# Optimization experiments

Hardware: AMD Instinct MI355X
Metric: run time of the kernel (lower is better)

The kernel has to match this reference:

```python
import jax, jax.numpy as jnp
import numpy as np

B, H, W, C = 4, 64, 64, 256
C8 = C // 8

def setup_inputs() -> dict:
    key = jax.random.key(0)
    k1, k2, k3, k4 = jax.random.split(key, 4)
    # glorot-uniform-ish init for 1x1 conv kernels stored as [Cin, Cout]
    def glorot(k, cin, cout):
        lim = np.sqrt(6.0 / (cin + cout)).astype(np.float32)
        return jax.random.uniform(k, (cin, cout), jnp.float32, -lim, lim)
    return {
        "x": jax.random.normal(k1, (B, H, W, C), jnp.float32),
        "kernel_f": glorot(k2, C, C8),
        "kernel_g": glorot(k3, C, C8),
        "kernel_h": glorot(k4, C, C),
        "gamma": jnp.zeros((1,), jnp.float32),
    }

def reference(x, kernel_f, kernel_g, kernel_h, gamma):
    b, h, w, c = x.shape
    n = h * w
    xf = x.reshape(b, n, c)                       # [B, N, C]
    # 1x1 convs == per-position matmuls
    f = jnp.einsum('bnc,cd->bnd', xf, kernel_f)   # [B, N, C/8]
    g = jnp.einsum('bnc,cd->bnd', xf, kernel_g)   # [B, N, C/8]
    hh = jnp.einsum('bnc,cd->bnd', xf, kernel_h)  # [B, N, C]
    s = jnp.einsum('bnd,bmd->bnm', g, f)          # [B, N, N]
    beta = jax.nn.softmax(s, axis=-1)
    o = jnp.einsum('bnm,bmc->bnc', beta, hh)      # [B, N, C]
    o = o.reshape(b, h, w, c)
    return gamma * o + x
```

## Files before the change

### kernel.cpp

```cpp
#include <hip/hip_runtime.h>
#include <hip/hip_bf16.h>

typedef __bf16 bf16x8 __attribute__((ext_vector_type(8)));
typedef float f32x4 __attribute__((ext_vector_type(4)));
typedef float f32x16 __attribute__((ext_vector_type(16)));
typedef unsigned short u16;
typedef unsigned int u32;
typedef const __attribute__((address_space(1))) u32 gu32;
typedef __attribute__((address_space(3))) u32 lu32;

__device__ __forceinline__ u16 f2bf_rne(float f){
  union { float f; u32 u; } v; v.f = f;
  u32 r = v.u + 0x7fffu + ((v.u >> 16) & 1u);
  return (u16)(r >> 16);
}
__device__ __forceinline__ u32 pack2(float a, float b){
  return __builtin_amdgcn_perm(__float_as_uint(a), __float_as_uint(b), 0x03020706u);
}
__device__ __forceinline__ void stage16(const u16* g, u16* l){
  __builtin_amdgcn_global_load_lds((gu32*)g, (lu32*)l, 16, 0, 0);
}
#define BARRIER_LGKM() asm volatile("s_waitcnt lgkmcnt(0)\n\ts_barrier" ::: "memory")

__global__ __launch_bounds__(256) void prep_kernel(
    const float* __restrict__ Wf, const float* __restrict__ Wg,
    const float* __restrict__ Wh, u16* __restrict__ WcatT){
  __shared__ float tile[32][33];
  const int tx = threadIdx.x & 31, ty = threadIdx.x >> 5;
  const int k0 = blockIdx.x * 32, n0 = blockIdx.y * 32;
  #pragma unroll
  for (int i = 0; i < 4; ++i){
    int k = k0 + ty + i * 8, n = n0 + tx;
    float v;
    if (n < 256)      v = Wh[k * 256 + n];
    else if (n < 288) v = Wf[k * 32 + (n - 256)];
    else              v = Wg[k * 32 + (n - 288)];
    tile[ty + i * 8][tx] = v;
  }
  __syncthreads();
  #pragma unroll
  for (int i = 0; i < 4; ++i){
    int n = n0 + ty + i * 8, k = k0 + tx;
    WcatT[n * 256 + k] = f2bf_rne(tile[tx][ty + i * 8]);
  }
}

__global__ __launch_bounds__(512) void proj_kernel(
    const float* __restrict__ x, const u16* __restrict__ WcatT,
    u16* __restrict__ Qg, u16* __restrict__ Kg, u16* __restrict__ Vfrag)
{
  __shared__ __align__(16) u16 smem[256 * 72];
  u16 (*xb)[264] = (u16(*)[264])smem;
  u16 (*Vr)[72]  = (u16(*)[72])smem;

  const int tid = threadIdx.x;
  const int lane = tid & 63, wave = tid >> 6;
  const int L = lane & 15, quad = lane >> 4;
  const int rowgrp = wave >> 1, colhalf = wave & 1;
  const int n0 = blockIdx.x * 64;

  const float4* xsrc = (const float4*)(x + (size_t)n0 * 256);
  #pragma unroll
  for (int j = 0; j < 8; ++j){
    int idx = j * 512 + tid;
    int row = idx >> 6, col4 = idx & 63;
    float4 v = xsrc[idx];
    u32 p0 = (u32)f2bf_rne(v.x) | ((u32)f2bf_rne(v.y) << 16);
    u32 p1 = (u32)f2bf_rne(v.z) | ((u32)f2bf_rne(v.w) << 16);
    *(uint2*)&xb[row][col4 * 4] = make_uint2(p0, p1);
  }
  __syncthreads();

  f32x4 acc[10];
  #pragma unroll
  for (int cc = 0; cc < 10; ++cc) acc[cc] = (f32x4){0.f, 0.f, 0.f, 0.f};

  #pragma unroll
  for (int kk = 0; kk < 8; ++kk){
    bf16x8 a = *(const bf16x8*)&xb[rowgrp * 16 + L][kk * 32 + quad * 8];
    #pragma unroll
    for (int cc = 0; cc < 10; ++cc){
      int ccg = colhalf * 10 + cc;
      bf16x8 bfr = *(const bf16x8*)(WcatT + (size_t)(ccg * 16 + L) * 256 + kk * 32 + quad * 8);
      acc[cc] = __builtin_amdgcn_mfma_f32_16x16x32_bf16(a, bfr, acc[cc], 0, 0, 0);
    }
  }

  if (colhalf){
    #pragma unroll
    for (int cc = 6; cc < 10; ++cc){
      int ccg = 10 + cc;
      u16* dst = (ccg < 18) ? Kg : Qg;
      float sc = (ccg < 18) ? 1.0f : 1.44269504088896f;
      int c = (ccg & 1) * 16 + L;
      #pragma unroll
      for (int r = 0; r < 4; ++r){
        int row = n0 + rowgrp * 16 + quad * 4 + r;
        dst[(size_t)row * 32 + c] = f2bf_rne(acc[cc][r] * sc);
      }
    }
  }

  __syncthreads();

  {
    const int cmax = colhalf ? 6 : 10;
    for (int cc = 0; cc < cmax; ++cc){
      int ccg = colhalf * 10 + cc;
      int c = ccg * 16 + L;
      #pragma unroll
      for (int r = 0; r < 4; ++r){
        int tn = rowgrp * 16 + quad * 4 + r;
        int p  = ((tn & 15) << 2) | (tn >> 4);
        Vr[c][p] = f2bf_rne(acc[cc][r]);
      }
    }
  }
  __syncthreads();

  u16* Vblk = Vfrag + (size_t)blockIdx.x * (256 * 64);
  #pragma unroll
  for (int i = 0; i < 4; ++i){
    int idx = i * 512 + tid;
    *(uint4*)(Vblk + (size_t)idx * 8) = *(const uint4*)&Vr[idx & 255][(idx >> 8) * 8];
  }
}

__global__ __launch_bounds__(512, 4) void flash_kernel(
    const u16* __restrict__ Qg, const u16* __restrict__ Kg, const u16* __restrict__ Vfrag,
    u16* __restrict__ Opart, float* __restrict__ Lpart)
{
  constexpr float SH = -92.33248261689366f;
  __shared__ __align__(16) u16 Plds[128][72];
  __shared__ __align__(16) u16 Vlds[16384];

  const int tid = threadIdx.x, lane = tid & 63, wave = tid >> 6;
  const int L = lane & 15, quad = lane >> 4;
  const int m32 = lane & 31, h32 = lane >> 5;
  const int qquad = wave & 3, chalf = wave >> 2;
  const int b = blockIdx.y, split = blockIdx.z;
  const int qblk = blockIdx.x * 128;

  const u16* Qb = Qg + (size_t)(b * 4096) * 32;
  const u16* Kb = Kg + (size_t)(b * 4096) * 32;
  const u16* Vb = Vfrag + (size_t)b * (64 * 256 * 64);

  const int g0 = split * 16;
  {
    const u16* vt = Vb + (size_t)g0 * (256 * 64);
    #pragma unroll
    for (int i = 0; i < 4; ++i){
      int chunk = wave * 4 + i;
      stage16(vt + chunk * 512 + lane * 8, &Vlds[chunk * 512]);
    }
  }
  bf16x8 qa = *(const bf16x8*)(Qb + (size_t)(qblk + wave * 16 + L) * 32 + quad * 8);
  const u16* kp0 = Kb + (size_t)(g0 * 64 + L) * 32 + quad * 8;
  bf16x8 kc0 = *(const bf16x8*)(kp0);
  bf16x8 kc1 = *(const bf16x8*)(kp0 + 512);
  bf16x8 kc2 = *(const bf16x8*)(kp0 + 1024);
  bf16x8 kc3 = *(const bf16x8*)(kp0 + 1536);

  f32x16 acc[4];
  #pragma unroll
  for (int ct = 0; ct < 4; ++ct)
    #pragma unroll
    for (int i = 0; i < 16; ++i) acc[ct][i] = 0.f;
  float lsum[4] = {0.f, 0.f, 0.f, 0.f};
  const f32x4 zero = (f32x4){0.f, 0.f, 0.f, 0.f};

  for (int kt = 0; kt < 16; ++kt){
    const int g = g0 + kt;

    f32x4 s0 = __builtin_amdgcn_mfma_f32_16x16x32_bf16(qa, kc0, zero, 0, 0, 0);
    f32x4 s1 = __builtin_amdgcn_mfma_f32_16x16x32_bf16(qa, kc1, zero, 0, 0, 0);
    f32x4 s2 = __builtin_amdgcn_mfma_f32_16x16x32_bf16(qa, kc2, zero, 0, 0, 0);
    f32x4 s3 = __builtin_amdgcn_mfma_f32_16x16x32_bf16(qa, kc3, zero, 0, 0, 0);

    #pragma unroll
    for (int r = 0; r < 4; ++r){
      float p0 = __builtin_amdgcn_exp2f(s0[r] + SH);
      float p1 = __builtin_amdgcn_exp2f(s1[r] + SH);
      float p2 = __builtin_amdgcn_exp2f(s2[r] + SH);
      float p3 = __builtin_amdgcn_exp2f(s3[r] + SH);
      lsum[r] += (p0 + p1) + (p2 + p3);
      *(uint2*)&Plds[wave * 16 + quad * 4 + r][L * 4] =
          make_uint2(pack2(p0, p1), pack2(p2, p3));
    }

    __syncthreads();

    bf16x8 kn0, kn1, kn2, kn3;
    if (kt < 15){
      const u16* kpn = Kb + (size_t)((g + 1) * 64 + L) * 32 + quad * 8;
      kn0 = *(const bf16x8*)(kpn);
      kn1 = *(const bf16x8*)(kpn + 512);
      kn2 = *(const bf16x8*)(kpn + 1024);
      kn3 = *(const bf16x8*)(kpn + 1536);
    }

    #pragma unroll
    for (int ks = 0; ks < 4; ++ks){
      bf16x8 af = *(const bf16x8*)&Plds[qquad * 32 + m32][ks * 16 + h32 * 8];
      const int vbase = ((ks * 2 + h32) * 256 + chalf * 128 + m32) * 8;
      #pragma unroll
      for (int ct = 0; ct < 4; ++ct){
        bf16x8 vf = *(const bf16x8*)&Vlds[vbase + ct * 32 * 8];
        acc[ct] = __builtin_amdgcn_mfma_f32_32x32x16_bf16(af, vf, acc[ct], 0, 0, 0);
      }
    }

    BARRIER_LGKM();

    if (kt < 15){
      const u16* vt = Vb + (size_t)(g + 1) * (256 * 64);
      #pragma unroll
      for (int i = 0; i < 4; ++i){
        int chunk = wave * 4 + i;
        stage16(vt + chunk * 512 + lane * 8, &Vlds[chunk * 512]);
      }
      kc0 = kn0; kc1 = kn1; kc2 = kn2; kc3 = kn3;
    }
  }

  u16* Ob = Opart + ((size_t)split * 16384 + (size_t)b * 4096 + qblk) * 256;
  #pragma unroll
  for (int ct = 0; ct < 4; ++ct){
    #pragma unroll
    for (int rg = 0; rg < 16; ++rg){
      int row = qquad * 32 + (rg & 3) + 8 * (rg >> 2) + 4 * h32;
      int c = chalf * 128 + ct * 32 + m32;
      Ob[(size_t)row * 256 + c] = (u16)(__float_as_uint(acc[ct][rg]) >> 16);
    }
  }
  #pragma unroll
  for (int r = 0; r < 4; ++r){
    lsum[r] += __shfl_xor(lsum[r], 1);
    lsum[r] += __shfl_xor(lsum[r], 2);
    lsum[r] += __shfl_xor(lsum[r], 4);
    lsum[r] += __shfl_xor(lsum[r], 8);
  }
  if (L == 0){
    float* Lp = Lpart + split * 16384 + b * 4096 + qblk + wave * 16;
    #pragma unroll
    for (int r = 0; r < 4; ++r) Lp[quad * 4 + r] = lsum[r];
  }
}

__global__ __launch_bounds__(256) void combine_kernel(
    const float* __restrict__ x, const float* __restrict__ gamma,
    const u16* __restrict__ Opart, const float* __restrict__ Lpart,
    float* __restrict__ out)
{
  const int t = threadIdx.x;
  const int row = blockIdx.x * 8 + (t >> 5);
  const int c0 = (t & 31) * 8;
  const size_t base = (size_t)row * 256 + c0;
  float os[8];
  #pragma unroll
  for (int i = 0; i < 8; ++i) os[i] = 0.f;
  float ls = 0.f;
  #pragma unroll
  for (int s = 0; s < 4; ++s){
    ls += Lpart[s * 16384 + row];
    uint4 u = *(const uint4*)(Opart + (size_t)s * 16384 * 256 + base);
    os[0] += __uint_as_float(u.x << 16);
    os[1] += __uint_as_float(u.x & 0xffff0000u);
    os[2] += __uint_as_float(u.y << 16);
    os[3] += __uint_as_float(u.y & 0xffff0000u);
    os[4] += __uint_as_float(u.z << 16);
    os[5] += __uint_as_float(u.z & 0xffff0000u);
    os[6] += __uint_as_float(u.w << 16);
    os[7] += __uint_as_float(u.w & 0xffff0000u);
  }
  const float r = gamma[0] / ls;
  float4 x0 = *(const float4*)(x + base);
  float4 x1 = *(const float4*)(x + base + 4);
  float4 o0, o1;
  o0.x = os[0] * r + x0.x;  o0.y = os[1] * r + x0.y;
  o0.z = os[2] * r + x0.z;  o0.w = os[3] * r + x0.w;
  o1.x = os[4] * r + x1.x;  o1.y = os[5] * r + x1.y;
  o1.z = os[6] * r + x1.z;  o1.w = os[7] * r + x1.w;
  *(float4*)(out + base)     = o0;
  *(float4*)(out + base + 4) = o1;
}

extern "C" void kernel_launch(void* const* d_in, const int* in_sizes, int n_in,
                              void* d_out, int out_size, void* d_ws, size_t ws_size,
                              hipStream_t stream) {
  const float* x     = (const float*)d_in[0];
  const float* Wf    = (const float*)d_in[1];
  const float* Wg    = (const float*)d_in[2];
  const float* Wh    = (const float*)d_in[3];
  const float* gamma = (const float*)d_in[4];
  float* out = (float*)d_out;

  u16* p = (u16*)d_ws;
  u16* Qg    = p;  p += 16384 * 32;
  u16* Kg    = p;  p += 16384 * 32;
  u16* Vfrag = p;  p += 4 * 64 * 256 * 64;
  u16* WcatT = p;  p += 320 * 256;
  u16* Opart = p;  p += (size_t)4 * 16384 * 256;
  float* Lpart = (float*)p;

  prep_kernel<<<dim3(8, 10), 256, 0, stream>>>(Wf, Wg, Wh, WcatT);
  proj_kernel<<<256, 512, 0, stream>>>(x, WcatT, Qg, Kg, Vfrag);
  flash_kernel<<<dim3(32, 4, 4), 512, 0, stream>>>(Qg, Kg, Vfrag, Opart, Lpart);
  combine_kernel<<<2048, 256, 0, stream>>>(x, gamma, Opart, Lpart, out);
}
```

Before: 161.0 us.

## Read V fragments straight from global and double-buffer P to drop a barrier

The flash kernel no longer stages each V tile into LDS via global_load_lds. Each wave now loads its V fragments directly from global memory, and its output tile changes from 32 rows × 128 columns to a 2×2 block of 64 rows × 64 columns. P goes into a double-buffered LDS array, so one barrier per iteration is enough instead of two, and the next-tile K loads are issued right after the QK MFMAs. This cuts LDS traffic and synchronisation but adds repeated global/L2 reads of V across waves and may expose global load latency ahead of the PV MFMAs.

```diff
diff --git a/kernel.cpp b/kernel.cpp
--- a/kernel.cpp
+++ b/kernel.cpp
@@ -6,8 +6,6 @@
 typedef float f32x16 __attribute__((ext_vector_type(16)));
 typedef unsigned short u16;
 typedef unsigned int u32;
-typedef const __attribute__((address_space(1))) u32 gu32;
-typedef __attribute__((address_space(3))) u32 lu32;
 
 __device__ __forceinline__ u16 f2bf_rne(float f){
   union { float f; u32 u; } v; v.f = f;
@@ -16,9 +14,6 @@
 }
 __device__ __forceinline__ u32 pack2(float a, float b){
   return __builtin_amdgcn_perm(__float_as_uint(a), __float_as_uint(b), 0x03020706u);
-}
-__device__ __forceinline__ void stage16(const u16* g, u16* l){
-  __builtin_amdgcn_global_load_lds((gu32*)g, (lu32*)l, 16, 0, 0);
 }
 #define BARRIER_LGKM() asm volatile("s_waitcnt lgkmcnt(0)\n\ts_barrier" ::: "memory")
 
@@ -131,13 +126,12 @@
     u16* __restrict__ Opart, float* __restrict__ Lpart)
 {
   constexpr float SH = -92.33248261689366f;
-  __shared__ __align__(16) u16 Plds[128][72];
-  __shared__ __align__(16) u16 Vlds[16384];
+  __shared__ __align__(16) u16 Plds[2][128][72];
 
   const int tid = threadIdx.x, lane = tid & 63, wave = tid >> 6;
   const int L = lane & 15, quad = lane >> 4;
   const int m32 = lane & 31, h32 = lane >> 5;
-  const int qquad = wave & 3, chalf = wave >> 2;
+  const int wq = wave >> 2, wc = wave & 3;
   const int b = blockIdx.y, split = blockIdx.z;
   const int qblk = blockIdx.x * 128;
 
@@ -146,14 +140,7 @@
   const u16* Vb = Vfrag + (size_t)b * (64 * 256 * 64);
 
   const int g0 = split * 16;
-  {
-    const u16* vt = Vb + (size_t)g0 * (256 * 64);
-    #pragma unroll
-    for (int i = 0; i < 4; ++i){
-      int chunk = wave * 4 + i;
-      stage16(vt + chunk * 512 + lane * 8, &Vlds[chunk * 512]);
-    }
-  }
+
   bf16x8 qa = *(const bf16x8*)(Qb + (size_t)(qblk + wave * 16 + L) * 32 + quad * 8);
   const u16* kp0 = Kb + (size_t)(g0 * 64 + L) * 32 + quad * 8;
   bf16x8 kc0 = *(const bf16x8*)(kp0);
@@ -163,19 +150,28 @@
 
   f32x16 acc[4];
   #pragma unroll
-  for (int ct = 0; ct < 4; ++ct)
-    #pragma unroll
-    for (int i = 0; i < 16; ++i) acc[ct][i] = 0.f;
+  for (int t = 0; t < 4; ++t)
+    #pragma unroll
+    for (int i = 0; i < 16; ++i) acc[t][i] = 0.f;
   float lsum[4] = {0.f, 0.f, 0.f, 0.f};
   const f32x4 zero = (f32x4){0.f, 0.f, 0.f, 0.f};
 
   for (int kt = 0; kt < 16; ++kt){
     const int g = g0 + kt;
+    u16 (*Pw)[72] = Plds[kt & 1];
 
     f32x4 s0 = __builtin_amdgcn_mfma_f32_16x16x32_bf16(qa, kc0, zero, 0, 0, 0);
     f32x4 s1 = __builtin_amdgcn_mfma_f32_16x16x32_bf16(qa, kc1, zero, 0, 0, 0);
     f32x4 s2 = __builtin_amdgcn_mfma_f32_16x16x32_bf16(qa, kc2, zero, 0, 0, 0);
     f32x4 s3 = __builtin_amdgcn_mfma_f32_16x16x32_bf16(qa, kc3, zero, 0, 0, 0);
+
+    if (kt < 15){
+      const u16* kpn = Kb + (size_t)((g + 1) * 64 + L) * 32 + quad * 8;
+      kc0 = *(const bf16x8*)(kpn);
+      kc1 = *(const bf16x8*)(kpn + 512);
+      kc2 = *(const bf16x8*)(kpn + 1024);
+      kc3 = *(const bf16x8*)(kpn + 1536);
+    }
 
     #pragma unroll
     for (int r = 0; r < 4; ++r){
@@ -184,53 +180,36 @@
       float p2 = __builtin_amdgcn_exp2f(s2[r] + SH);
       float p3 = __builtin_amdgcn_exp2f(s3[r] + SH);
       lsum[r] += (p0 + p1) + (p2 + p3);
-      *(uint2*)&Plds[wave * 16 + quad * 4 + r][L * 4] =
+      *(uint2*)&Pw[wave * 16 + quad * 4 + r][L * 4] =
           make_uint2(pack2(p0, p1), pack2(p2, p3));
     }
 
-    __syncthreads();
-
-    bf16x8 kn0, kn1, kn2, kn3;
-    if (kt < 15){
-      const u16* kpn = Kb + (size_t)((g + 1) * 64 + L) * 32 + quad * 8;
-      kn0 = *(const bf16x8*)(kpn);
-      kn1 = *(const bf16x8*)(kpn + 512);
-      kn2 = *(const bf16x8*)(kpn + 1024);
-      kn3 = *(const bf16x8*)(kpn + 1536);
-    }
-
+    BARRIER_LGKM();
+
+    const u16* Vtile = Vb + (size_t)g * (256 * 64);
     #pragma unroll
     for (int ks = 0; ks < 4; ++ks){
-      bf16x8 af = *(const bf16x8*)&Plds[qquad * 32 + m32][ks * 16 + h32 * 8];
-      const int vbase = ((ks * 2 + h32) * 256 + chalf * 128 + m32) * 8;
-      #pragma unroll
-      for (int ct = 0; ct < 4; ++ct){
-        bf16x8 vf = *(const bf16x8*)&Vlds[vbase + ct * 32 * 8];
-        acc[ct] = __builtin_amdgcn_mfma_f32_32x32x16_bf16(af, vf, acc[ct], 0, 0, 0);
-      }
-    }
-
-    BARRIER_LGKM();
-
-    if (kt < 15){
-      const u16* vt = Vb + (size_t)(g + 1) * (256 * 64);
-      #pragma unroll
-      for (int i = 0; i < 4; ++i){
-        int chunk = wave * 4 + i;
-        stage16(vt + chunk * 512 + lane * 8, &Vlds[chunk * 512]);
-      }
-      kc0 = kn0; kc1 = kn1; kc2 = kn2; kc3 = kn3;
+      const u16* vrow = Vtile + (size_t)((ks * 2 + h32) * 256 + wc * 64 + m32) * 8;
+      bf16x8 vf0 = *(const bf16x8*)(vrow);
+      bf16x8 vf1 = *(const bf16x8*)(vrow + 32 * 8);
+      bf16x8 af0 = *(const bf16x8*)&Pw[wq * 64 + m32][ks * 16 + h32 * 8];
+      bf16x8 af1 = *(const bf16x8*)&Pw[wq * 64 + 32 + m32][ks * 16 + h32 * 8];
+      acc[0] = __builtin_amdgcn_mfma_f32_32x32x16_bf16(af0, vf0, acc[0], 0, 0, 0);
+      acc[1] = __builtin_amdgcn_mfma_f32_32x32x16_bf16(af0, vf1, acc[1], 0, 0, 0);
+      acc[2] = __builtin_amdgcn_mfma_f32_32x32x16_bf16(af1, vf0, acc[2], 0, 0, 0);
+      acc[3] = __builtin_amdgcn_mfma_f32_32x32x16_bf16(af1, vf1, acc[3], 0, 0, 0);
     }
   }
 
   u16* Ob = Opart + ((size_t)split * 16384 + (size_t)b * 4096 + qblk) * 256;
   #pragma unroll
-  for (int ct = 0; ct < 4; ++ct){
+  for (int t = 0; t < 4; ++t){
+    const int qi = t >> 1, ci = t & 1;
     #pragma unroll
     for (int rg = 0; rg < 16; ++rg){
-      int row = qquad * 32 + (rg & 3) + 8 * (rg >> 2) + 4 * h32;
-      int c = chalf * 128 + ct * 32 + m32;
-      Ob[(size_t)row * 256 + c] = (u16)(__float_as_uint(acc[ct][rg]) >> 16);
+      int row = wq * 64 + qi * 32 + (rg & 3) + 8 * (rg >> 2) + 4 * h32;
+      int c = wc * 64 + ci * 32 + m32;
+      Ob[(size_t)row * 256 + c] = (u16)(__float_as_uint(acc[t][rg]) >> 16);
     }
   }
   #pragma unroll
```

After: 168.8 us. 4.8% more time.
